# Kernel tuning notes

Measured on AMD Instinct MI355X. Metric: run time of the kernel, lower is better.

## Reference

```python
import jax, jax.numpy as jnp
import numpy as np

N = 500_000          # nodes
E = 8_000_000        # edges (avg degree 16)
C = 2                # in/out channels
STEP_DIM = 8
NUM_STEPS = 100
K = 2                # k_hops -> powers [0, 1]
HID = 8              # hidden_layers


def setup_inputs() -> dict:
    key = jax.random.key(0)
    ks = jax.random.split(key, 6)
    X = jax.random.normal(ks[0], (N, C), dtype=jnp.float32)
    edge_index = jax.random.randint(ks[1], (2, E), 0, N, dtype=jnp.int32)
    step_emb = jax.random.normal(ks[2], (NUM_STEPS, STEP_DIM), dtype=jnp.float32)
    d_in0 = C + STEP_DIM  # 10
    # layer 0: one Linear per power p in {0,1}
    W0 = jax.random.normal(ks[3], (K, d_in0, C), dtype=jnp.float32) / np.sqrt(d_in0).astype(np.float32)
    b0 = jnp.zeros((K, C), dtype=jnp.float32)
    # layers 1..7, stacked for lax.scan
    Wh = jax.random.normal(ks[4], (HID - 1, K, C, C), dtype=jnp.float32) / np.sqrt(C).astype(np.float32)
    bh = jnp.zeros((HID - 1, K, C), dtype=jnp.float32)
    return dict(X=X, edge_index=edge_index, step_index=7, step_emb=step_emb,
                W0=W0, b0=b0, Wh=Wh, bh=bh)


def _make_prop(edge_index, n):
    """GCN-normalized propagation with self-loops (PyG gcn_norm), as used by MixHopConv."""
    src, dst = edge_index[0], edge_index[1]
    # in-degree on destination nodes, +1 for the self-loop
    deg = jnp.zeros((n,), jnp.float32).at[dst].add(1.0) + 1.0
    dis = jax.lax.rsqrt(deg)  # deg^{-1/2}; deg >= 1 so no inf handling needed
    edge_w = dis[src] * dis[dst]  # [E]

    def prop(x):
        msg = x[src] * edge_w[:, None]                      # [E, F] gather
        out = jax.ops.segment_sum(msg, dst, num_segments=n)  # [N, F] scatter-add
        return out + x * (dis * dis)[:, None]               # self-loop term
    return prop


def reference(X, edge_index, step_index, step_emb, W0, b0, Wh, bh):
    n = X.shape[0]
    prop = _make_prop(edge_index, n)

    s = jnp.broadcast_to(step_emb[step_index], (n, STEP_DIM))
    x = jnp.concatenate([X, s], axis=-1)  # [N, 10]

    # layer 0: concat(xW0, (Ax)W1) -> view(-1,K,C).sum(1) -> relu  ==  relu(xW0+b0 + (Ax)W1+b1)
    x = jax.nn.relu(x @ W0[0] + b0[0] + prop(x) @ W0[1] + b0[1])  # [N, 2]

    def body(x, wb):
        W, b = wb  # W: [K, C, C], b: [K, C]
        h = x @ W[0] + b[0] + prop(x) @ W[1] + b[1]
        return jax.nn.relu(h), None

    x, _ = jax.lax.scan(body, x, (Wh, bh))
    return x
```

## Files before the change

kernel.cpp:

```cpp
#include <hip/hip_runtime.h>


constexpr int NN = 500000;
constexpr int NE = 8000000;
constexpr int STEP_DIM = 8;
constexpr int HIDM1 = 7;

constexpr int BSH  = 9;
constexpr int BNOD = 1 << BSH;
constexpr int NBUK = (NN + BNOD - 1) / BNOD;
constexpr int NBLK = 125;
constexpr int EPB  = NE / NBLK;
constexpr int QPB  = EPB / 4;

constexpr int SLOT  = 9216;
constexpr int CPT   = SLOT / 512;
constexpr int WSPAN = 64 * CPT;
constexpr unsigned SENT = (unsigned)BNOD << 19;

typedef unsigned u32x4 __attribute__((ext_vector_type(4)));
typedef unsigned u32x2 __attribute__((ext_vector_type(2)));

__device__ __forceinline__ int swiz(int L) {
  int w = L / WSPAN;
  int r = L - w * WSPAN;
  int l = r / CPT;
  int o = r - l * CPT;
  int base = w * WSPAN;
  return (o < 16) ? base + (o >> 2) * 256 + l * 4 + (o & 3)
                  : base + 1024 + l * 2 + (o - 16);
}


__global__ __launch_bounds__(1024) void k_bhist(const int* __restrict__ dst,
                                                int* __restrict__ bhist) {
  __shared__ int hist[NBUK];
  int b = blockIdx.x, t = threadIdx.x;
  for (int h = t; h < NBUK; h += 1024) hist[h] = 0;
  __syncthreads();
  const int4* d4p = (const int4*)dst + (size_t)b * QPB;
  for (int i = t; i < QPB; i += 1024) {
    int4 d = d4p[i];
    atomicAdd(&hist[d.x >> BSH], 1);
    atomicAdd(&hist[d.y >> BSH], 1);
    atomicAdd(&hist[d.z >> BSH], 1);
    atomicAdd(&hist[d.w >> BSH], 1);
  }
  __syncthreads();
  for (int h = t; h < NBUK; h += 1024) bhist[h * NBLK + b] = hist[h];
}


__global__ __launch_bounds__(128) void k_rowscan(int* __restrict__ bhist,
                                                 int* __restrict__ bcount) {
  __shared__ int sm[128];
  int h = blockIdx.x, t = threadIdx.x;
  int v = (t < NBLK) ? bhist[h * NBLK + t] : 0;
  sm[t] = v;
  __syncthreads();
  for (int o = 1; o < 128; o <<= 1) {
    int x = (t >= o) ? sm[t - o] : 0;
    __syncthreads();
    sm[t] += x;
    __syncthreads();
  }
  if (t < NBLK) bhist[h * NBLK + t] = sm[t] - v;
  if (t == 127) bcount[h] = sm[127];
}


__global__ __launch_bounds__(1024) void k_bscatter(const int* __restrict__ src,
                                                   const int* __restrict__ dst,
                                                   const int* __restrict__ off,
                                                   unsigned int* __restrict__ col2) {
  __shared__ int cur[NBUK];
  int b = blockIdx.x, t = threadIdx.x;
  for (int h = t; h < NBUK; h += 1024) cur[h] = h * SLOT + off[h * NBLK + b];
  __syncthreads();
  const int4* s4p = (const int4*)src + (size_t)b * QPB;
  const int4* d4p = (const int4*)dst + (size_t)b * QPB;
  for (int i = t; i < QPB; i += 1024) {
    int4 s = s4p[i];
    int4 d = d4p[i];
    int p0 = atomicAdd(&cur[d.x >> BSH], 1);
    col2[p0] = ((unsigned)(d.x & (BNOD - 1)) << 19) | (unsigned)s.x;
    int p1 = atomicAdd(&cur[d.y >> BSH], 1);
    col2[p1] = ((unsigned)(d.y & (BNOD - 1)) << 19) | (unsigned)s.y;
    int p2 = atomicAdd(&cur[d.z >> BSH], 1);
    col2[p2] = ((unsigned)(d.z & (BNOD - 1)) << 19) | (unsigned)s.z;
    int p3 = atomicAdd(&cur[d.w >> BSH], 1);
    col2[p3] = ((unsigned)(d.w & (BNOD - 1)) << 19) | (unsigned)s.w;
  }
}


__global__ __launch_bounds__(512) void k_sort(unsigned int* __restrict__ col2,
                                              const int* __restrict__ bcount,
                                              const float2* __restrict__ X,
                                              float* __restrict__ dis,
                                              float2* __restrict__ xs0) {
  __shared__ unsigned stage[SLOT];
  __shared__ int hist[BNOD];
  __shared__ int tsum[512];
  int b = blockIdx.x, t = threadIdx.x;
  int ns = bcount[b];
  if (ns > SLOT) ns = SLOT;
  unsigned* base = col2 + (size_t)b * SLOT;
  hist[t] = 0;
  __syncthreads();
  for (int i = t; i < ns; i += 512) {
    unsigned p = base[i];
    stage[i] = p;
    atomicAdd(&hist[p >> 19], 1);
  }
  __syncthreads();
  int a = hist[t];
  tsum[t] = a;
  __syncthreads();
  for (int o = 1; o < 512; o <<= 1) {
    int v = (t >= o) ? tsum[t - o] : 0;
    __syncthreads();
    tsum[t] += v;
    __syncthreads();
  }
  hist[t] = tsum[t] - a;
  __syncthreads();
  for (int i = t; i < ns; i += 512) {
    unsigned p = stage[i];
    int pos = atomicAdd(&hist[p >> 19], 1);
    base[swiz(pos)] = p;
  }
  for (int L = ns + t; L < SLOT; L += 512) base[swiz(L)] = SENT;
  int i = (b << BSH) + t;
  if (i < NN) {
    float d = rsqrtf((float)a + 1.0f);
    dis[i] = d;
    float2 x = X[i];
    xs0[i] = make_float2(d * x.x, d * x.y);
  }
}


__global__ __launch_bounds__(512) void k_blayer0(const unsigned int* __restrict__ col2,
                                                 const float2* __restrict__ xs0,
                                                 const float2* __restrict__ X,
                                                 const float* __restrict__ dis,
                                                 const float* __restrict__ W0,
                                                 const float* __restrict__ b0,
                                                 const float* __restrict__ step_emb,
                                                 const int* __restrict__ step_index,
                                                 float2* __restrict__ xs_out) {
  __shared__ float acc[(BNOD + 1) * 3];
  int b = blockIdx.x, t = threadIdx.x;
  for (int j = t; j < (BNOD + 1) * 3; j += 512) acc[j] = 0.f;
  __syncthreads();
  const unsigned* bp = col2 + (size_t)b * SLOT + (t >> 6) * WSPAN;
  int l = t & 63;
  int cur = BNOD;
  float rx = 0.f, ry = 0.f, rd = 0.f;
  unsigned ebuf[CPT];
#pragma unroll
  for (int i = 0; i < 4; ++i) {
    u32x4 q = __builtin_nontemporal_load((const u32x4*)(bp + i * 256 + l * 4));
#pragma unroll
    for (int j = 0; j < 4; ++j) ebuf[i * 4 + j] = q[j];
  }
  {
    u32x2 q2 = __builtin_nontemporal_load((const u32x2*)(bp + 1024 + l * 2));
    ebuf[16] = q2[0];
    ebuf[17] = q2[1];
  }
#pragma unroll
  for (int o = 0; o < CPT; ++o) {
    unsigned p = ebuf[o];
    int s = p & 0x7FFFF;
    float2 v = xs0[s];
    float dv = dis[s];
    int ld = (int)(p >> 19);
    if (ld != cur) {
      atomicAdd(&acc[cur * 3 + 0], rx);
      atomicAdd(&acc[cur * 3 + 1], ry);
      atomicAdd(&acc[cur * 3 + 2], rd);
      cur = ld;
      rx = v.x; ry = v.y; rd = dv;
    } else {
      rx += v.x; ry += v.y; rd += dv;
    }
  }
  atomicAdd(&acc[cur * 3 + 0], rx);
  atomicAdd(&acc[cur * 3 + 1], ry);
  atomicAdd(&acc[cur * 3 + 2], rd);
  __syncthreads();
  const float* sv = step_emb + step_index[0] * STEP_DIM;
  float c0[2], c1[2];
#pragma unroll
  for (int o = 0; o < 2; ++o) {
    float a0 = b0[o] + b0[2 + o];
    float a1 = 0.f;
#pragma unroll
    for (int j = 0; j < STEP_DIM; ++j) {
      a0 += sv[j] * W0[(2 + j) * 2 + o];
      a1 += sv[j] * W0[20 + (2 + j) * 2 + o];
    }
    c0[o] = a0;
    c1[o] = a1;
  }
  int i = (b << BSH) + t;
  if (i < NN) {
    float d = dis[i], d2 = d * d;
    float2 x = X[i];
    float px = d * acc[t * 3 + 0] + d2 * x.x;
    float py = d * acc[t * 3 + 1] + d2 * x.y;
    float rowsum = d * acc[t * 3 + 2] + d2;
    float h0 = c0[0] + rowsum * c1[0] + x.x * W0[0] + x.y * W0[2] + px * W0[20] + py * W0[22];
    float h1 = c0[1] + rowsum * c1[1] + x.x * W0[1] + x.y * W0[3] + px * W0[21] + py * W0[23];
    h0 = fmaxf(h0, 0.f);
    h1 = fmaxf(h1, 0.f);
    xs_out[i] = make_float2(d * h0, d * h1);
  }
}

__global__ __launch_bounds__(512) void k_blayer(const unsigned int* __restrict__ col2,
                                                const float* __restrict__ dis,
                                                const float2* __restrict__ xs_in,
                                                const float* __restrict__ W,
                                                const float* __restrict__ bb,
                                                float2* __restrict__ xs_out,
                                                float2* __restrict__ out,
                                                int last) {
  __shared__ float acc[(BNOD + 1) * 2];
  int b = blockIdx.x, t = threadIdx.x;
  for (int j = t; j < (BNOD + 1) * 2; j += 512) acc[j] = 0.f;
  __syncthreads();
  const unsigned* bp = col2 + (size_t)b * SLOT + (t >> 6) * WSPAN;
  int l = t & 63;
  int cur = BNOD;
  float rx = 0.f, ry = 0.f;
  unsigned ebuf[CPT];
#pragma unroll
  for (int i = 0; i < 4; ++i) {
    u32x4 q = __builtin_nontemporal_load((const u32x4*)(bp + i * 256 + l * 4));
#pragma unroll
    for (int j = 0; j < 4; ++j) ebuf[i * 4 + j] = q[j];
  }
  {
    u32x2 q2 = __builtin_nontemporal_load((const u32x2*)(bp + 1024 + l * 2));
    ebuf[16] = q2[0];
    ebuf[17] = q2[1];
  }
#pragma unroll
  for (int o = 0; o < CPT; ++o) {
    unsigned p = ebuf[o];
    float2 v = xs_in[p & 0x7FFFF];
    int ld = (int)(p >> 19);
    if (ld != cur) {
      atomicAdd(&acc[cur * 2 + 0], rx);
      atomicAdd(&acc[cur * 2 + 1], ry);
      cur = ld;
      rx = v.x; ry = v.y;
    } else {
      rx += v.x; ry += v.y;
    }
  }
  atomicAdd(&acc[cur * 2 + 0], rx);
  atomicAdd(&acc[cur * 2 + 1], ry);
  __syncthreads();
  int i = (b << BSH) + t;
  if (i < NN) {
    float d = dis[i];
    float2 xsv = xs_in[i];
    float inv = 1.0f / d;
    float xx = xsv.x * inv, xy = xsv.y * inv;
    float px = d * (acc[t * 2 + 0] + xsv.x);
    float py = d * (acc[t * 2 + 1] + xsv.y);
    float h0 = bb[0] + bb[2] + xx * W[0] + xy * W[2] + px * W[4] + py * W[6];
    float h1 = bb[1] + bb[3] + xx * W[1] + xy * W[3] + px * W[5] + py * W[7];
    h0 = fmaxf(h0, 0.f);
    h1 = fmaxf(h1, 0.f);
    if (last) {
      out[i] = make_float2(h0, h1);
    } else {
      xs_out[i] = make_float2(d * h0, d * h1);
    }
  }
}


extern "C" void kernel_launch(void* const* d_in, const int* in_sizes, int n_in,
                              void* d_out, int out_size, void* d_ws, size_t ws_size,
                              hipStream_t stream) {
  const float2* X        = (const float2*)d_in[0];
  const int*    edge     = (const int*)d_in[1];
  const int*    src      = edge;
  const int*    dstp     = edge + NE;
  const int*    step_idx = (const int*)d_in[2];
  const float*  step_emb = (const float*)d_in[3];
  const float*  W0       = (const float*)d_in[4];
  const float*  b0       = (const float*)d_in[5];
  const float*  Wh       = (const float*)d_in[6];
  const float*  bbias    = (const float*)d_in[7];

  int*      ip     = (int*)d_ws;
  unsigned* col2   = (unsigned*)ip;
  size_t    o      = (size_t)NBUK * SLOT;
  int*      bhist  = ip + o;            o += 122128;
  int*      bcount = ip + o;            o += 1024;
  float*    dis    = (float*)(ip + o);  o += 500224;
  float2*   bufA   = (float2*)(ip + o); o += 2 * 500224;
  float2*   bufB   = (float2*)(ip + o);

  k_bhist<<<NBLK, 1024, 0, stream>>>(dstp, bhist);
  k_rowscan<<<NBUK, 128, 0, stream>>>(bhist, bcount);
  k_bscatter<<<NBLK, 1024, 0, stream>>>(src, dstp, bhist, col2);
  k_sort<<<NBUK, 512, 0, stream>>>(col2, bcount, X, dis, bufA);

  k_blayer0<<<NBUK, 512, 0, stream>>>(col2, bufA, X, dis, W0, b0,
                                      step_emb, step_idx, bufB);
  float2* cur = bufB;
  float2* nxt = bufA;
  for (int l = 0; l < HIDM1; ++l) {
    k_blayer<<<NBUK, 512, 0, stream>>>(col2, dis, cur, Wh + l * 8,
                                       bbias + l * 4, nxt, (float2*)d_out,
                                       l == HIDM1 - 1 ? 1 : 0);
    float2* tmp = cur;
    cur = nxt;
    nxt = tmp;
  }
}
```

Before: 679.0 us.

## Replace global bucket scatter with per-block LDS local sort and gather

Adds a new preprocessing path: 500 blocks each histogram and locally sort their edge chunk by destination bucket in shared memory, then write the result contiguously with nontemporal stores together with per-block bucket start offsets. A second kernel gathers each bucket's segments from all 500 blocks into LDS and finishes the within-bucket sort. This replaces the histogram, row-scan and scattered-atomic-write kernels, aiming to cut one pass over dst and the scattered global writes. The new path needs extra workspace and falls back to the old path if the workspace is too small. It also trades those writes for per-thread serial segment copies in the gather kernel, which may be uncoalesced.

```diff
diff --git a/kernel.cpp b/kernel.cpp
--- a/kernel.cpp
+++ b/kernel.cpp
@@ -9,14 +9,19 @@
 constexpr int BSH  = 9;
 constexpr int BNOD = 1 << BSH;
 constexpr int NBUK = (NN + BNOD - 1) / BNOD;
-constexpr int NBLK = 125;
-constexpr int EPB  = NE / NBLK;
-constexpr int QPB  = EPB / 4;
-
 constexpr int SLOT  = 9216;
 constexpr int CPT   = SLOT / 512;
 constexpr int WSPAN = 64 * CPT;
 constexpr unsigned SENT = (unsigned)BNOD << 19;
+
+constexpr int PA_NBLK = 500;
+constexpr int PA_EPB  = NE / PA_NBLK;
+constexpr int PA_QPB  = PA_EPB / 4;
+constexpr int PA_SC   = NBUK + 1;
+
+constexpr int PB_NBLK = 125;
+constexpr int PB_EPB  = NE / PB_NBLK;
+constexpr int PB_QPB  = PB_EPB / 4;
 
 typedef unsigned u32x4 __attribute__((ext_vector_type(4)));
 typedef unsigned u32x2 __attribute__((ext_vector_type(2)));
@@ -32,14 +37,19 @@
 }
 
 
-__global__ __launch_bounds__(1024) void k_bhist(const int* __restrict__ dst,
-                                                int* __restrict__ bhist) {
+__global__ __launch_bounds__(512) void k_lsort(const int* __restrict__ src,
+                                               const int* __restrict__ dst,
+                                               unsigned* __restrict__ colraw,
+                                               int* __restrict__ starts2) {
+  __shared__ unsigned stage[PA_EPB];
   __shared__ int hist[NBUK];
-  int b = blockIdx.x, t = threadIdx.x;
-  for (int h = t; h < NBUK; h += 1024) hist[h] = 0;
-  __syncthreads();
-  const int4* d4p = (const int4*)dst + (size_t)b * QPB;
-  for (int i = t; i < QPB; i += 1024) {
+  __shared__ int tsum[512];
+  int b = blockIdx.x, t = threadIdx.x;
+  for (int h = t; h < NBUK; h += 512) hist[h] = 0;
+  __syncthreads();
+  const int4* d4p = (const int4*)dst + (size_t)b * PA_QPB;
+  const int4* s4p = (const int4*)src + (size_t)b * PA_QPB;
+  for (int i = t; i < PA_QPB; i += 512) {
     int4 d = d4p[i];
     atomicAdd(&hist[d.x >> BSH], 1);
     atomicAdd(&hist[d.y >> BSH], 1);
@@ -47,15 +57,142 @@
     atomicAdd(&hist[d.w >> BSH], 1);
   }
   __syncthreads();
-  for (int h = t; h < NBUK; h += 1024) bhist[h * NBLK + b] = hist[h];
-}
-
-
-__global__ __launch_bounds__(128) void k_rowscan(int* __restrict__ bhist,
-                                                 int* __restrict__ bcount) {
+  int h0 = 2 * t, h1 = 2 * t + 1;
+  int a0 = (h0 < NBUK) ? hist[h0] : 0;
+  int a1 = (h1 < NBUK) ? hist[h1] : 0;
+  tsum[t] = a0 + a1;
+  __syncthreads();
+  for (int o = 1; o < 512; o <<= 1) {
+    int v = (t >= o) ? tsum[t - o] : 0;
+    __syncthreads();
+    tsum[t] += v;
+    __syncthreads();
+  }
+  int ex = tsum[t] - (a0 + a1);
+  __syncthreads();
+  if (h0 < NBUK) hist[h0] = ex;
+  if (h1 < NBUK) hist[h1] = ex + a0;
+  __syncthreads();
+  int* st = starts2 + (size_t)b * PA_SC;
+  for (int h = t; h < NBUK; h += 512) st[h] = hist[h];
+  if (t == 0) st[NBUK] = PA_EPB;
+  __syncthreads();
+  for (int i = t; i < PA_QPB; i += 512) {
+    int4 d = d4p[i];
+    int4 s = s4p[i];
+    int p0 = atomicAdd(&hist[d.x >> BSH], 1);
+    stage[p0] = ((unsigned)(d.x & (BNOD - 1)) << 19) | (unsigned)s.x;
+    int p1 = atomicAdd(&hist[d.y >> BSH], 1);
+    stage[p1] = ((unsigned)(d.y & (BNOD - 1)) << 19) | (unsigned)s.y;
+    int p2 = atomicAdd(&hist[d.z >> BSH], 1);
+    stage[p2] = ((unsigned)(d.z & (BNOD - 1)) << 19) | (unsigned)s.z;
+    int p3 = atomicAdd(&hist[d.w >> BSH], 1);
+    stage[p3] = ((unsigned)(d.w & (BNOD - 1)) << 19) | (unsigned)s.w;
+  }
+  __syncthreads();
+  u32x4* out4 = (u32x4*)(colraw + (size_t)b * PA_EPB);
+  for (int i = t; i < PA_QPB; i += 512) {
+    u32x4 q;
+    q[0] = stage[4 * i + 0];
+    q[1] = stage[4 * i + 1];
+    q[2] = stage[4 * i + 2];
+    q[3] = stage[4 * i + 3];
+    __builtin_nontemporal_store(q, out4 + i);
+  }
+}
+
+
+__global__ __launch_bounds__(512) void k_sortA(const unsigned* __restrict__ colraw,
+                                               const int* __restrict__ starts2,
+                                               unsigned* __restrict__ col2,
+                                               const float2* __restrict__ X,
+                                               float* __restrict__ dis,
+                                               float2* __restrict__ xs0) {
+  __shared__ unsigned stage[SLOT];
+  __shared__ int hist[BNOD];
+  __shared__ int tsum[512];
+  __shared__ int nsh;
+  int h = blockIdx.x, t = threadIdx.x;
+  int s = 0, len = 0;
+  if (t < PA_NBLK) {
+    s = starts2[(size_t)t * PA_SC + h];
+    int e = starts2[(size_t)t * PA_SC + h + 1];
+    len = e - s;
+  }
+  tsum[t] = len;
+  __syncthreads();
+  for (int o = 1; o < 512; o <<= 1) {
+    int v = (t >= o) ? tsum[t - o] : 0;
+    __syncthreads();
+    tsum[t] += v;
+    __syncthreads();
+  }
+  int pos = tsum[t] - len;
+  if (t == 511) nsh = tsum[511];
+  __syncthreads();
+  int ns = nsh;
+  if (ns > SLOT) ns = SLOT;
+  const unsigned* rw = colraw + (size_t)t * PA_EPB + s;
+  for (int j = 0; j < len; ++j) {
+    int p = pos + j;
+    if (p < SLOT) stage[p] = rw[j];
+  }
+  __syncthreads();
+  hist[t] = 0;
+  __syncthreads();
+  for (int i = t; i < ns; i += 512) atomicAdd(&hist[stage[i] >> 19], 1);
+  __syncthreads();
+  int a = hist[t];
+  tsum[t] = a;
+  __syncthreads();
+  for (int o = 1; o < 512; o <<= 1) {
+    int v = (t >= o) ? tsum[t - o] : 0;
+    __syncthreads();
+    tsum[t] += v;
+    __syncthreads();
+  }
+  hist[t] = tsum[t] - a;
+  __syncthreads();
+  unsigned* base = col2 + (size_t)h * SLOT;
+  for (int i = t; i < ns; i += 512) {
+    unsigned p = stage[i];
+    int pp = atomicAdd(&hist[p >> 19], 1);
+    base[swiz(pp)] = p;
+  }
+  for (int L = ns + t; L < SLOT; L += 512) base[swiz(L)] = SENT;
+  int i = (h << BSH) + t;
+  if (i < NN) {
+    float d = rsqrtf((float)a + 1.0f);
+    dis[i] = d;
+    float2 x = X[i];
+    xs0[i] = make_float2(d * x.x, d * x.y);
+  }
+}
+
+
+__global__ __launch_bounds__(1024) void k_bhistB(const int* __restrict__ dst,
+                                                 int* __restrict__ bhist) {
+  __shared__ int hist[NBUK];
+  int b = blockIdx.x, t = threadIdx.x;
+  for (int h = t; h < NBUK; h += 1024) hist[h] = 0;
+  __syncthreads();
+  const int4* d4p = (const int4*)dst + (size_t)b * PB_QPB;
+  for (int i = t; i < PB_QPB; i += 1024) {
+    int4 d = d4p[i];
+    atomicAdd(&hist[d.x >> BSH], 1);
+    atomicAdd(&hist[d.y >> BSH], 1);
+    atomicAdd(&hist[d.z >> BSH], 1);
+    atomicAdd(&hist[d.w >> BSH], 1);
+  }
+  __syncthreads();
+  for (int h = t; h < NBUK; h += 1024) bhist[h * PB_NBLK + b] = hist[h];
+}
+
+__global__ __launch_bounds__(128) void k_rowscanB(int* __restrict__ bhist,
+                                                  int* __restrict__ bcount) {
   __shared__ int sm[128];
   int h = blockIdx.x, t = threadIdx.x;
-  int v = (t < NBLK) ? bhist[h * NBLK + t] : 0;
+  int v = (t < PB_NBLK) ? bhist[h * PB_NBLK + t] : 0;
   sm[t] = v;
   __syncthreads();
   for (int o = 1; o < 128; o <<= 1) {
@@ -64,22 +201,21 @@
     sm[t] += x;
     __syncthreads();
   }
-  if (t < NBLK) bhist[h * NBLK + t] = sm[t] - v;
+  if (t < PB_NBLK) bhist[h * PB_NBLK + t] = sm[t] - v;
   if (t == 127) bcount[h] = sm[127];
 }
 
-
-__global__ __launch_bounds__(1024) void k_bscatter(const int* __restrict__ src,
-                                                   const int* __restrict__ dst,
-                                                   const int* __restrict__ off,
-                                                   unsigned int* __restrict__ col2) {
+__global__ __launch_bounds__(1024) void k_bscatterB(const int* __restrict__ src,
+                                                    const int* __restrict__ dst,
+                                                    const int* __restrict__ off,
+                                                    unsigned int* __restrict__ col2) {
   __shared__ int cur[NBUK];
   int b = blockIdx.x, t = threadIdx.x;
-  for (int h = t; h < NBUK; h += 1024) cur[h] = h * SLOT + off[h * NBLK + b];
-  __syncthreads();
-  const int4* s4p = (const int4*)src + (size_t)b * QPB;
-  const int4* d4p = (const int4*)dst + (size_t)b * QPB;
-  for (int i = t; i < QPB; i += 1024) {
+  for (int h = t; h < NBUK; h += 1024) cur[h] = h * SLOT + off[h * PB_NBLK + b];
+  __syncthreads();
+  const int4* s4p = (const int4*)src + (size_t)b * PB_QPB;
+  const int4* d4p = (const int4*)dst + (size_t)b * PB_QPB;
+  for (int i = t; i < PB_QPB; i += 1024) {
     int4 s = s4p[i];
     int4 d = d4p[i];
     int p0 = atomicAdd(&cur[d.x >> BSH], 1);
@@ -93,12 +229,11 @@
   }
 }
 
-
-__global__ __launch_bounds__(512) void k_sort(unsigned int* __restrict__ col2,
-                                              const int* __restrict__ bcount,
-                                              const float2* __restrict__ X,
-                                              float* __restrict__ dis,
-                                              float2* __restrict__ xs0) {
+__global__ __launch_bounds__(512) void k_sortB(unsigned int* __restrict__ col2,
+                                               const int* __restrict__ bcount,
+                                               const float2* __restrict__ X,
+                                               float* __restrict__ dis,
+                                               float2* __restrict__ xs0) {
   __shared__ unsigned stage[SLOT];
   __shared__ int hist[BNOD];
   __shared__ int tsum[512];
@@ -300,19 +435,33 @@
   const float*  Wh       = (const float*)d_in[6];
   const float*  bbias    = (const float*)d_in[7];
 
-  int*      ip     = (int*)d_ws;
-  unsigned* col2   = (unsigned*)ip;
-  size_t    o      = (size_t)NBUK * SLOT;
-  int*      bhist  = ip + o;            o += 122128;
-  int*      bcount = ip + o;            o += 1024;
-  float*    dis    = (float*)(ip + o);  o += 500224;
-  float2*   bufA   = (float2*)(ip + o); o += 2 * 500224;
-  float2*   bufB   = (float2*)(ip + o);
-
-  k_bhist<<<NBLK, 1024, 0, stream>>>(dstp, bhist);
-  k_rowscan<<<NBUK, 128, 0, stream>>>(bhist, bcount);
-  k_bscatter<<<NBLK, 1024, 0, stream>>>(src, dstp, bhist, col2);
-  k_sort<<<NBUK, 512, 0, stream>>>(col2, bcount, X, dis, bufA);
+  int*      ip   = (int*)d_ws;
+  unsigned* col2 = (unsigned*)ip;
+  size_t    o    = (size_t)NBUK * SLOT;
+
+  size_t oA = o;
+  unsigned* colraw  = (unsigned*)(ip + oA);  oA += NE;
+  int*      starts2 = ip + oA;               oA += ((size_t)PA_NBLK * PA_SC + 8) & ~3;
+  size_t oB = o;
+  int*      bhist   = ip + oB;               oB += ((size_t)NBUK * PB_NBLK + 8) & ~3;
+  int*      bcount  = ip + oB;               oB += 1024;
+
+  size_t tail = (size_t)500224 + 2 * 1000448 + 1000448;
+  bool pathA = ws_size >= (oA + tail) * sizeof(int);
+  size_t ot = pathA ? oA : oB;
+  float*  dis  = (float*)(ip + ot);   ot += 500224;
+  float2* bufA = (float2*)(ip + ot);  ot += 2 * 500224;
+  float2* bufB = (float2*)(ip + ot);
+
+  if (pathA) {
+    k_lsort<<<PA_NBLK, 512, 0, stream>>>(src, dstp, colraw, starts2);
+    k_sortA<<<NBUK, 512, 0, stream>>>(colraw, starts2, col2, X, dis, bufA);
+  } else {
+    k_bhistB<<<PB_NBLK, 1024, 0, stream>>>(dstp, bhist);
+    k_rowscanB<<<NBUK, 128, 0, stream>>>(bhist, bcount);
+    k_bscatterB<<<PB_NBLK, 1024, 0, stream>>>(src, dstp, bhist, col2);
+    k_sortB<<<NBUK, 512, 0, stream>>>(col2, bcount, X, dis, bufA);
+  }
 
   k_blayer0<<<NBUK, 512, 0, stream>>>(col2, bufA, X, dis, W0, b0,
                                       step_emb, step_idx, bufB);
```

Result: faster. 659.1 us (-2.9%).
